# Kernel optimization log

Hardware: AMD Instinct MI355X
Metric: run time of the kernel (lower is better)

Reference implementation:

```python
import math
import jax, jax.numpy as jnp
import numpy as np

B, S, D_MODEL, NUM_HEADS = 4, 2048, 1024, 16
D_N = D_MODEL // NUM_HEADS  # 64


def setup_inputs() -> dict:
    key = jax.random.key(0)
    ks = jax.random.split(key, 10)
    scale = 1.0 / math.sqrt(D_MODEL)
    return {
        "q": jax.random.normal(ks[0], (B, S, D_MODEL), dtype=jnp.float32),
        "k": jax.random.normal(ks[1], (B, S, D_MODEL), dtype=jnp.float32),
        "v": jax.random.normal(ks[2], (B, S, D_MODEL), dtype=jnp.float32),
        "mask": jax.random.uniform(ks[3], (B, S, S), dtype=jnp.float32),
        "w_q": jax.random.normal(ks[4], (D_N, D_MODEL), dtype=jnp.float32) * scale,
        "b_q": jnp.zeros((D_N,), dtype=jnp.float32),
        "w_k": jax.random.normal(ks[5], (D_N, D_MODEL), dtype=jnp.float32) * scale,
        "b_k": jnp.zeros((D_N,), dtype=jnp.float32),
        "w_v": jax.random.normal(ks[6], (D_N, D_MODEL), dtype=jnp.float32) * scale,
        "b_v": jnp.zeros((D_N,), dtype=jnp.float32),
    }


def reference(q, k, v, mask, w_q, b_q, w_k, b_k, w_v, b_v):
    # Linear projections d_model -> d_n (torch Linear: x @ W.T + b)
    qp = jnp.einsum("bsd,nd->bsn", q, w_q) + b_q  # [B,S,d_n]
    kp = jnp.einsum("bsd,nd->bsn", k, w_k) + b_k
    vp = jnp.einsum("bsd,nd->bsn", v, w_v) + b_v
    # Scaled dot-product scores with additive mask penalty
    scores = jnp.einsum("bqn,bkn->bqk", qp, kp) / math.sqrt(D_N) + mask * (-1e9)
    attn = jax.nn.softmax(scores, axis=-1)  # [B,S,S]
    return jnp.einsum("bqk,bkn->bqn", attn, vp)  # [B,S,d_n]
```

## Files before the change

### kernel.cpp

```cpp
#include <hip/hip_runtime.h>
#include <hip/hip_bf16.h>

#define BB 4
#define SS 2048
#define DM 1024
#define DN 64

typedef short short8 __attribute__((ext_vector_type(8)));
typedef float f32x4 __attribute__((ext_vector_type(4)));
typedef unsigned short ushort;

__device__ __forceinline__ ushort f2bf(float f) {
    union { float f; unsigned u; } v; v.f = f;
    unsigned r = v.u + 0x7fffu + ((v.u >> 16) & 1u);
    return (ushort)(r >> 16);
}
__device__ __forceinline__ float bf2f(ushort h) {
    union { unsigned u; float f; } v; v.u = ((unsigned)h) << 16; return v.f;
}

__global__ __launch_bounds__(256) void prep_w(
    const float* __restrict__ wq, const float* __restrict__ wk,
    const float* __restrict__ wv, ushort* __restrict__ w_bf)
{
    int i = blockIdx.x * 256 + threadIdx.x;
    int p = i >> 14;
    int j = (i & 16383) * 4;
    const float* src = (p == 0) ? wq : (p == 1) ? wk : wv;
    float4 f = *(const float4*)(src + j);
    ushort o[4] = { f2bf(f.x), f2bf(f.y), f2bf(f.z), f2bf(f.w) };
    *(unsigned long long*)(w_bf + p * 65536 + j) = *(unsigned long long*)o;
}

__global__ __launch_bounds__(128, 2) void proj_kernel(
    const float* __restrict__ q, const float* __restrict__ k, const float* __restrict__ v,
    const ushort* __restrict__ w_bf,
    const float* __restrict__ bq, const float* __restrict__ bk, const float* __restrict__ bvp,
    ushort* __restrict__ qp, ushort* __restrict__ kp, ushort* __restrict__ vpT)
{
    const int tid  = threadIdx.x;
    const int proj = blockIdx.y;
    const int wv_id = tid >> 6;
    const int lane  = tid & 63;
    const int l16   = lane & 15;
    const int quad  = lane >> 4;
    const int g     = blockIdx.x * 2 + wv_id;
    const int m0    = g * 16;

    const float* x     = (proj == 0) ? q  : (proj == 1) ? k  : v;
    const ushort* wb   = w_bf + proj * 65536;
    const float* bias  = (proj == 0) ? bq : (proj == 1) ? bk : bvp;

    const float* arow = x + (size_t)(m0 + l16) * DM + quad * 8;

    f32x4 acc[4];
#pragma unroll
    for (int t = 0; t < 4; t++) acc[t] = (f32x4){0.f, 0.f, 0.f, 0.f};

#pragma unroll 4
    for (int kb = 0; kb < DM; kb += 32) {
        float4 f0 = *(const float4*)(arow + kb);
        float4 f1 = *(const float4*)(arow + kb + 4);
        ushort ta[8] = { f2bf(f0.x), f2bf(f0.y), f2bf(f0.z), f2bf(f0.w),
                         f2bf(f1.x), f2bf(f1.y), f2bf(f1.z), f2bf(f1.w) };
        short8 a = *(short8*)ta;
#pragma unroll
        for (int t = 0; t < 4; t++) {
            short8 b = *(const short8*)(wb + (size_t)(t * 16 + l16) * DM + kb + quad * 8);
            acc[t] = __builtin_amdgcn_mfma_f32_16x16x32_bf16(a, b, acc[t], 0, 0, 0);
        }
    }

#pragma unroll
    for (int t = 0; t < 4; t++) {
        int n = t * 16 + l16;
        float bb_ = bias[n];
#pragma unroll
        for (int r = 0; r < 4; r++) {
            int grow = m0 + quad * 4 + r;
            ushort h = f2bf(acc[t][r] + bb_);
            if (proj == 0)      qp[(size_t)grow * DN + n] = h;
            else if (proj == 1) kp[(size_t)grow * DN + n] = h;
            else {
                int bb = grow >> 11, s = grow & 2047;
                vpT[((size_t)bb * DN + n) * SS + s] = h;
            }
        }
    }
}

template<int KPS>
__global__ __launch_bounds__(256, 2) void flash_kernel(
    const float* __restrict__ mask,
    const ushort* __restrict__ qp,
    const ushort* __restrict__ kp,
    const ushort* __restrict__ vpT,
    ushort* __restrict__ part_O,
    float* __restrict__ part_ml)
{
    constexpr int NSLICE = SS / KPS;
    constexpr int NIT    = KPS / 64;

    __shared__ __align__(16) ushort p_lds[4][16][72];

    const int tid  = threadIdx.x;
    const int wv   = tid >> 6;
    const int lane = tid & 63;
    const int l16  = lane & 15;
    const int quad = lane >> 4;

    const int gw    = blockIdx.x * 4 + wv;
    const int qg    = gw & 127;
    const int rest  = gw >> 7;
    const int slice = rest % NSLICE;
    const int b     = rest / NSLICE;

    const ushort* qbase = qp + ((size_t)b * SS + qg * 16 + l16) * DN + quad * 8;
    short8 aq0 = *(const short8*)(qbase);
    short8 aq1 = *(const short8*)(qbase + 32);

    float m_r[4] = { -__builtin_inff(), -__builtin_inff(),
                     -__builtin_inff(), -__builtin_inff() };
    float l_r[4] = { 0.f, 0.f, 0.f, 0.f };
    f32x4 Oacc[4];
#pragma unroll
    for (int t = 0; t < 4; t++) Oacc[t] = (f32x4){0.f, 0.f, 0.f, 0.f};

    const size_t mrow0 = ((size_t)b * SS + qg * 16 + quad * 4) * SS;
    const int k_begin = slice * KPS;

    float  mk[2][4][4];
    short8 bk0[2][4], bk1[2][4];

    auto load_tile = [&](int buf, int k0) {
#pragma unroll
        for (int t = 0; t < 4; t++) {
            const ushort* kb_ = kp + ((size_t)b * SS + k0 + t * 16 + l16) * DN + quad * 8;
            bk0[buf][t] = *(const short8*)(kb_);
            bk1[buf][t] = *(const short8*)(kb_ + 32);
        }
#pragma unroll
        for (int t = 0; t < 4; t++)
#pragma unroll
            for (int r = 0; r < 4; r++)
                mk[buf][t][r] = mask[mrow0 + (size_t)r * SS + k0 + t * 16 + l16];
    };

    load_tile(0, k_begin);

#pragma unroll
    for (int it = 0; it < NIT; ++it) {
        const int cur = it & 1;
        const int k0  = k_begin + it * 64;

        if (it + 1 < NIT) load_tile(cur ^ 1, k0 + 64);

        short8 bv0[4], bv1[4];
#pragma unroll
        for (int tf = 0; tf < 4; tf++) {
            const ushort* vb_ = vpT + ((size_t)b * DN + tf * 16 + l16) * SS + k0 + quad * 8;
            bv0[tf] = *(const short8*)(vb_);
            bv1[tf] = *(const short8*)(vb_ + 32);
        }

        f32x4 sc[4];
#pragma unroll
        for (int t = 0; t < 4; t++) {
            f32x4 z = (f32x4){0.f, 0.f, 0.f, 0.f};
            z = __builtin_amdgcn_mfma_f32_16x16x32_bf16(aq0, bk0[cur][t], z, 0, 0, 0);
            z = __builtin_amdgcn_mfma_f32_16x16x32_bf16(aq1, bk1[cur][t], z, 0, 0, 0);
            sc[t] = z;
        }

#pragma unroll
        for (int r = 0; r < 4; r++) {
            float s[4];
            float tmax = -__builtin_inff();
#pragma unroll
            for (int t = 0; t < 4; t++) {
                s[t] = sc[t][r] * 0.125f - 1e9f * mk[cur][t][r];
                tmax = fmaxf(tmax, s[t]);
            }
#pragma unroll
            for (int off = 8; off >= 1; off >>= 1)
                tmax = fmaxf(tmax, __shfl_xor(tmax, off, 16));
            float mnew  = fmaxf(m_r[r], tmax);
            float alpha = __expf(m_r[r] - mnew);
            m_r[r] = mnew;
            float rs = 0.f;
#pragma unroll
            for (int t = 0; t < 4; t++) {
                float pv = __expf(s[t] - mnew);
                rs += pv;
                p_lds[wv][quad * 4 + r][t * 16 + l16] = f2bf(pv);
            }
#pragma unroll
            for (int off = 8; off >= 1; off >>= 1)
                rs += __shfl_xor(rs, off, 16);
            l_r[r] = l_r[r] * alpha + rs;
#pragma unroll
            for (int tf = 0; tf < 4; tf++)
                Oacc[tf][r] *= alpha;
        }

        short8 ap0 = *(const short8*)&p_lds[wv][l16][quad * 8];
        short8 ap1 = *(const short8*)&p_lds[wv][l16][32 + quad * 8];
#pragma unroll
        for (int tf = 0; tf < 4; tf++) {
            Oacc[tf] = __builtin_amdgcn_mfma_f32_16x16x32_bf16(ap0, bv0[tf], Oacc[tf], 0, 0, 0);
            Oacc[tf] = __builtin_amdgcn_mfma_f32_16x16x32_bf16(ap1, bv1[tf], Oacc[tf], 0, 0, 0);
        }
    }

    const int rowg = (b * SS + qg * 16) + quad * 4;
#pragma unroll
    for (int r = 0; r < 4; r++) {
        size_t row = (size_t)rowg + r;
        if (l16 == 0) {
            part_ml[((size_t)slice * (BB * SS) + row) * 2 + 0] = m_r[r];
            part_ml[((size_t)slice * (BB * SS) + row) * 2 + 1] = l_r[r];
        }
#pragma unroll
        for (int tf = 0; tf < 4; tf++)
            part_O[((size_t)slice * (BB * SS) + row) * DN + tf * 16 + l16] =
                f2bf(Oacc[tf][r]);
    }
}

__global__ __launch_bounds__(256) void combine_kernel(
    const ushort* __restrict__ part_O, const float* __restrict__ part_ml,
    float* __restrict__ out, int nslice)
{
    const int tid = threadIdx.x;
    const int row = blockIdx.x * 4 + (tid >> 6);
    const int f   = tid & 63;

    float ms[8], ls[8];
    float M = -__builtin_inff();
    for (int i = 0; i < nslice; i++) {
        ms[i] = part_ml[((size_t)i * (BB * SS) + row) * 2 + 0];
        ls[i] = part_ml[((size_t)i * (BB * SS) + row) * 2 + 1];
        M = fmaxf(M, ms[i]);
    }
    float L = 0.f, acc = 0.f;
    for (int i = 0; i < nslice; i++) {
        float e = __expf(ms[i] - M);
        L += e * ls[i];
        acc += e * bf2f(part_O[((size_t)i * (BB * SS) + row) * DN + f]);
    }
    out[(size_t)row * DN + f] = acc / L;
}

extern "C" void kernel_launch(void* const* d_in, const int* in_sizes, int n_in,
                              void* d_out, int out_size, void* d_ws, size_t ws_size,
                              hipStream_t stream) {
    const float* q    = (const float*)d_in[0];
    const float* k    = (const float*)d_in[1];
    const float* v    = (const float*)d_in[2];
    const float* mask = (const float*)d_in[3];
    const float* wq   = (const float*)d_in[4];
    const float* bq   = (const float*)d_in[5];
    const float* wk   = (const float*)d_in[6];
    const float* bk   = (const float*)d_in[7];
    const float* wv   = (const float*)d_in[8];
    const float* bv   = (const float*)d_in[9];
    float* out = (float*)d_out;

    char* p = (char*)d_ws;
    ushort* w_bf = (ushort*)p;                 p += 3 * 65536 * sizeof(ushort);
    ushort* qp   = (ushort*)p;                 p += (size_t)BB * SS * DN * 2;
    ushort* kp   = (ushort*)p;                 p += (size_t)BB * SS * DN * 2;
    ushort* vpT  = (ushort*)p;                 p += (size_t)BB * SS * DN * 2;
    size_t fixed = (size_t)(p - (char*)d_ws);

    int split = 8;
    while (split > 1 &&
           fixed + (size_t)split * ((size_t)BB * SS * 2 * 4 + (size_t)BB * SS * DN * 2) > ws_size)
        split >>= 1;

    float*  part_ml = (float*)p;               p += (size_t)split * BB * SS * 2 * 4;
    ushort* part_O  = (ushort*)p;

    prep_w<<<192, 256, 0, stream>>>(wq, wk, wv, w_bf);
    proj_kernel<<<dim3(256, 3), 128, 0, stream>>>(q, k, v, w_bf, bq, bk, bv, qp, kp, vpT);
    switch (split) {
        case 8:  flash_kernel<256> <<<128 * 8, 256, 0, stream>>>(mask, qp, kp, vpT, part_O, part_ml); break;
        case 4:  flash_kernel<512> <<<128 * 4, 256, 0, stream>>>(mask, qp, kp, vpT, part_O, part_ml); break;
        case 2:  flash_kernel<1024><<<128 * 2, 256, 0, stream>>>(mask, qp, kp, vpT, part_O, part_ml); break;
        default: flash_kernel<2048><<<128 * 1, 256, 0, stream>>>(mask, qp, kp, vpT, part_O, part_ml); break;
    }
    combine_kernel<<<(BB * SS) / 4, 256, 0, stream>>>(part_O, part_ml, out, split);
}
```

Measured before the change: 240.1 us.

## Fuse split-K combine into flash kernel and drop weight prep kernel

Removes the separate weight bf16 conversion kernel: the projection kernel now reads fp32 weights directly, truncates them to bf16, and software-prefetches its A and B operands. The flash kernel now assigns four key slices to the four waves of one block. It stages mask tiles through LDS with coalesced float4 loads and merges the partial softmax results in shared memory, so the partial-output buffers and the combine kernel are gone. The goal is fewer launches, less global traffic for partials, and better mask load coalescing. The cost is fewer flash blocks (512), which lowers parallelism, plus truncation rounding on the weights.

```diff
diff --git a/kernel.cpp b/kernel.cpp
--- a/kernel.cpp
+++ b/kernel.cpp
@@ -15,59 +15,95 @@
     unsigned r = v.u + 0x7fffu + ((v.u >> 16) & 1u);
     return (ushort)(r >> 16);
 }
-__device__ __forceinline__ float bf2f(ushort h) {
-    union { unsigned u; float f; } v; v.u = ((unsigned)h) << 16; return v.f;
-}
-
-__global__ __launch_bounds__(256) void prep_w(
-    const float* __restrict__ wq, const float* __restrict__ wk,
-    const float* __restrict__ wv, ushort* __restrict__ w_bf)
-{
-    int i = blockIdx.x * 256 + threadIdx.x;
-    int p = i >> 14;
-    int j = (i & 16383) * 4;
-    const float* src = (p == 0) ? wq : (p == 1) ? wk : wv;
-    float4 f = *(const float4*)(src + j);
-    ushort o[4] = { f2bf(f.x), f2bf(f.y), f2bf(f.z), f2bf(f.w) };
-    *(unsigned long long*)(w_bf + p * 65536 + j) = *(unsigned long long*)o;
-}
-
-__global__ __launch_bounds__(128, 2) void proj_kernel(
+__device__ __forceinline__ ushort f2bf_t(float f) {
+    union { float f; unsigned u; } v; v.f = f;
+    return (ushort)(v.u >> 16);
+}
+__device__ __forceinline__ short8 cvt8_rtn(float4 a, float4 b) {
+    ushort t[8] = { f2bf(a.x), f2bf(a.y), f2bf(a.z), f2bf(a.w),
+                    f2bf(b.x), f2bf(b.y), f2bf(b.z), f2bf(b.w) };
+    return *(short8*)t;
+}
+__device__ __forceinline__ short8 cvt8_trc(float4 a, float4 b) {
+    ushort t[8] = { f2bf_t(a.x), f2bf_t(a.y), f2bf_t(a.z), f2bf_t(a.w),
+                    f2bf_t(b.x), f2bf_t(b.y), f2bf_t(b.z), f2bf_t(b.w) };
+    return *(short8*)t;
+}
+
+__global__ __launch_bounds__(256) void proj_kernel(
     const float* __restrict__ q, const float* __restrict__ k, const float* __restrict__ v,
-    const ushort* __restrict__ w_bf,
+    const float* __restrict__ wq, const float* __restrict__ wk, const float* __restrict__ wvm,
     const float* __restrict__ bq, const float* __restrict__ bk, const float* __restrict__ bvp,
     ushort* __restrict__ qp, ushort* __restrict__ kp, ushort* __restrict__ vpT)
 {
-    const int tid  = threadIdx.x;
-    const int proj = blockIdx.y;
+    const int tid   = threadIdx.x;
     const int wv_id = tid >> 6;
     const int lane  = tid & 63;
     const int l16   = lane & 15;
     const int quad  = lane >> 4;
-    const int g     = blockIdx.x * 2 + wv_id;
-    const int m0    = g * 16;
-
-    const float* x     = (proj == 0) ? q  : (proj == 1) ? k  : v;
-    const ushort* wb   = w_bf + proj * 65536;
-    const float* bias  = (proj == 0) ? bq : (proj == 1) ? bk : bvp;
+    const int w     = blockIdx.x * 4 + wv_id;
+    const int proj  = w >> 9;
+    const int m0    = (w & 511) << 4;
+
+    const float* x    = (proj == 0) ? q  : (proj == 1) ? k  : v;
+    const float* wm   = (proj == 0) ? wq : (proj == 1) ? wk : wvm;
+    const float* bias = (proj == 0) ? bq : (proj == 1) ? bk : bvp;
 
     const float* arow = x + (size_t)(m0 + l16) * DM + quad * 8;
+    const float* brow0 = wm + (size_t)(l16     ) * DM + quad * 8;
+    const float* brow1 = wm + (size_t)(l16 + 16) * DM + quad * 8;
+    const float* brow2 = wm + (size_t)(l16 + 32) * DM + quad * 8;
+    const float* brow3 = wm + (size_t)(l16 + 48) * DM + quad * 8;
+
+    float4 apf[4][2];
+    float4 bpf[2][4][2];
+#pragma unroll
+    for (int i = 0; i < 4; i++) {
+        apf[i][0] = *(const float4*)(arow + i * 32);
+        apf[i][1] = *(const float4*)(arow + i * 32 + 4);
+    }
+#pragma unroll
+    for (int i = 0; i < 2; i++) {
+        bpf[i][0][0] = *(const float4*)(brow0 + i * 32);
+        bpf[i][0][1] = *(const float4*)(brow0 + i * 32 + 4);
+        bpf[i][1][0] = *(const float4*)(brow1 + i * 32);
+        bpf[i][1][1] = *(const float4*)(brow1 + i * 32 + 4);
+        bpf[i][2][0] = *(const float4*)(brow2 + i * 32);
+        bpf[i][2][1] = *(const float4*)(brow2 + i * 32 + 4);
+        bpf[i][3][0] = *(const float4*)(brow3 + i * 32);
+        bpf[i][3][1] = *(const float4*)(brow3 + i * 32 + 4);
+    }
 
     f32x4 acc[4];
 #pragma unroll
     for (int t = 0; t < 4; t++) acc[t] = (f32x4){0.f, 0.f, 0.f, 0.f};
 
-#pragma unroll 4
-    for (int kb = 0; kb < DM; kb += 32) {
-        float4 f0 = *(const float4*)(arow + kb);
-        float4 f1 = *(const float4*)(arow + kb + 4);
-        ushort ta[8] = { f2bf(f0.x), f2bf(f0.y), f2bf(f0.z), f2bf(f0.w),
-                         f2bf(f1.x), f2bf(f1.y), f2bf(f1.z), f2bf(f1.w) };
-        short8 a = *(short8*)ta;
-#pragma unroll
-        for (int t = 0; t < 4; t++) {
-            short8 b = *(const short8*)(wb + (size_t)(t * 16 + l16) * DM + kb + quad * 8);
-            acc[t] = __builtin_amdgcn_mfma_f32_16x16x32_bf16(a, b, acc[t], 0, 0, 0);
+#pragma unroll
+    for (int c = 0; c < 32; c++) {
+        const int ai = c & 3, bi = c & 1;
+        short8 a  = cvt8_rtn(apf[ai][0], apf[ai][1]);
+        short8 b0 = cvt8_trc(bpf[bi][0][0], bpf[bi][0][1]);
+        short8 b1 = cvt8_trc(bpf[bi][1][0], bpf[bi][1][1]);
+        short8 b2 = cvt8_trc(bpf[bi][2][0], bpf[bi][2][1]);
+        short8 b3 = cvt8_trc(bpf[bi][3][0], bpf[bi][3][1]);
+        acc[0] = __builtin_amdgcn_mfma_f32_16x16x32_bf16(a, b0, acc[0], 0, 0, 0);
+        acc[1] = __builtin_amdgcn_mfma_f32_16x16x32_bf16(a, b1, acc[1], 0, 0, 0);
+        acc[2] = __builtin_amdgcn_mfma_f32_16x16x32_bf16(a, b2, acc[2], 0, 0, 0);
+        acc[3] = __builtin_amdgcn_mfma_f32_16x16x32_bf16(a, b3, acc[3], 0, 0, 0);
+        if (c + 4 < 32) {
+            apf[ai][0] = *(const float4*)(arow + (c + 4) * 32);
+            apf[ai][1] = *(const float4*)(arow + (c + 4) * 32 + 4);
+        }
+        if (c + 2 < 32) {
+            const int kb = (c + 2) * 32;
+            bpf[bi][0][0] = *(const float4*)(brow0 + kb);
+            bpf[bi][0][1] = *(const float4*)(brow0 + kb + 4);
+            bpf[bi][1][0] = *(const float4*)(brow1 + kb);
+            bpf[bi][1][1] = *(const float4*)(brow1 + kb + 4);
+            bpf[bi][2][0] = *(const float4*)(brow2 + kb);
+            bpf[bi][2][1] = *(const float4*)(brow2 + kb + 4);
+            bpf[bi][3][0] = *(const float4*)(brow3 + kb);
+            bpf[bi][3][1] = *(const float4*)(brow3 + kb + 4);
         }
     }
 
@@ -82,42 +118,53 @@
             if (proj == 0)      qp[(size_t)grow * DN + n] = h;
             else if (proj == 1) kp[(size_t)grow * DN + n] = h;
             else {
-                int bb = grow >> 11, s = grow & 2047;
-                vpT[((size_t)bb * DN + n) * SS + s] = h;
+                int bb = grow >> 11, ss = grow & 2047;
+                vpT[((size_t)bb * DN + n) * SS + ss] = h;
             }
         }
     }
 }
 
-template<int KPS>
 __global__ __launch_bounds__(256, 2) void flash_kernel(
     const float* __restrict__ mask,
     const ushort* __restrict__ qp,
     const ushort* __restrict__ kp,
     const ushort* __restrict__ vpT,
-    ushort* __restrict__ part_O,
-    float* __restrict__ part_ml)
+    float* __restrict__ out)
 {
-    constexpr int NSLICE = SS / KPS;
-    constexpr int NIT    = KPS / 64;
-
-    __shared__ __align__(16) ushort p_lds[4][16][72];
+    __shared__ __align__(16) char smem[4 * 6656];
 
     const int tid  = threadIdx.x;
     const int wv   = tid >> 6;
     const int lane = tid & 63;
     const int l16  = lane & 15;
     const int quad = lane >> 4;
-
-    const int gw    = blockIdx.x * 4 + wv;
-    const int qg    = gw & 127;
-    const int rest  = gw >> 7;
-    const int slice = rest % NSLICE;
-    const int b     = rest / NSLICE;
+    const int b    = blockIdx.x >> 7;
+    const int qg   = blockIdx.x & 127;
+
+    float*  maskb = (float*)(smem + wv * 6656);
+    ushort* pbuf  = (ushort*)(smem + wv * 6656 + 4352);
+
+    const int k_begin = wv * 512;
 
     const ushort* qbase = qp + ((size_t)b * SS + qg * 16 + l16) * DN + quad * 8;
     short8 aq0 = *(const short8*)(qbase);
     short8 aq1 = *(const short8*)(qbase + 32);
+
+    const int mrow = lane >> 2;
+    const int mseg = lane & 3;
+    const float* mg = mask + ((size_t)b * SS + qg * 16 + mrow) * SS + mseg * 4;
+    float4 mpf[4];
+#pragma unroll
+    for (int j = 0; j < 4; j++) mpf[j] = *(const float4*)(mg + k_begin + j * 16);
+
+    short8 bk0[4], bk1[4];
+#pragma unroll
+    for (int t = 0; t < 4; t++) {
+        const ushort* p_ = kp + ((size_t)b * SS + k_begin + t * 16 + l16) * DN + quad * 8;
+        bk0[t] = *(const short8*)p_;
+        bk1[t] = *(const short8*)(p_ + 32);
+    }
 
     float m_r[4] = { -__builtin_inff(), -__builtin_inff(),
                      -__builtin_inff(), -__builtin_inff() };
@@ -126,59 +173,51 @@
 #pragma unroll
     for (int t = 0; t < 4; t++) Oacc[t] = (f32x4){0.f, 0.f, 0.f, 0.f};
 
-    const size_t mrow0 = ((size_t)b * SS + qg * 16 + quad * 4) * SS;
-    const int k_begin = slice * KPS;
-
-    float  mk[2][4][4];
-    short8 bk0[2][4], bk1[2][4];
-
-    auto load_tile = [&](int buf, int k0) {
-#pragma unroll
-        for (int t = 0; t < 4; t++) {
-            const ushort* kb_ = kp + ((size_t)b * SS + k0 + t * 16 + l16) * DN + quad * 8;
-            bk0[buf][t] = *(const short8*)(kb_);
-            bk1[buf][t] = *(const short8*)(kb_ + 32);
-        }
-#pragma unroll
-        for (int t = 0; t < 4; t++)
-#pragma unroll
-            for (int r = 0; r < 4; r++)
-                mk[buf][t][r] = mask[mrow0 + (size_t)r * SS + k0 + t * 16 + l16];
-    };
-
-    load_tile(0, k_begin);
-
-#pragma unroll
-    for (int it = 0; it < NIT; ++it) {
-        const int cur = it & 1;
-        const int k0  = k_begin + it * 64;
-
-        if (it + 1 < NIT) load_tile(cur ^ 1, k0 + 64);
+#pragma unroll
+    for (int it = 0; it < 8; ++it) {
+        const int k0 = k_begin + it * 64;
+
+#pragma unroll
+        for (int j = 0; j < 4; j++)
+            *(float4*)(maskb + mrow * 68 + j * 16 + mseg * 4) = mpf[j];
+        if (it < 7) {
+#pragma unroll
+            for (int j = 0; j < 4; j++) mpf[j] = *(const float4*)(mg + k0 + 64 + j * 16);
+        }
 
         short8 bv0[4], bv1[4];
 #pragma unroll
         for (int tf = 0; tf < 4; tf++) {
-            const ushort* vb_ = vpT + ((size_t)b * DN + tf * 16 + l16) * SS + k0 + quad * 8;
-            bv0[tf] = *(const short8*)(vb_);
-            bv1[tf] = *(const short8*)(vb_ + 32);
+            const ushort* p_ = vpT + ((size_t)b * DN + tf * 16 + l16) * SS + k0 + quad * 8;
+            bv0[tf] = *(const short8*)p_;
+            bv1[tf] = *(const short8*)(p_ + 32);
         }
 
         f32x4 sc[4];
 #pragma unroll
         for (int t = 0; t < 4; t++) {
             f32x4 z = (f32x4){0.f, 0.f, 0.f, 0.f};
-            z = __builtin_amdgcn_mfma_f32_16x16x32_bf16(aq0, bk0[cur][t], z, 0, 0, 0);
-            z = __builtin_amdgcn_mfma_f32_16x16x32_bf16(aq1, bk1[cur][t], z, 0, 0, 0);
+            z = __builtin_amdgcn_mfma_f32_16x16x32_bf16(aq0, bk0[t], z, 0, 0, 0);
+            z = __builtin_amdgcn_mfma_f32_16x16x32_bf16(aq1, bk1[t], z, 0, 0, 0);
             sc[t] = z;
         }
+        if (it < 7) {
+#pragma unroll
+            for (int t = 0; t < 4; t++) {
+                const ushort* p_ = kp + ((size_t)b * SS + k0 + 64 + t * 16 + l16) * DN + quad * 8;
+                bk0[t] = *(const short8*)p_;
+                bk1[t] = *(const short8*)(p_ + 32);
+            }
+        }
 
 #pragma unroll
         for (int r = 0; r < 4; r++) {
+            const float* mrow_l = maskb + (quad * 4 + r) * 68;
             float s[4];
             float tmax = -__builtin_inff();
 #pragma unroll
             for (int t = 0; t < 4; t++) {
-                s[t] = sc[t][r] * 0.125f - 1e9f * mk[cur][t][r];
+                s[t] = sc[t][r] * 0.125f - 1e9f * mrow_l[t * 16 + l16];
                 tmax = fmaxf(tmax, s[t]);
             }
 #pragma unroll
@@ -192,7 +231,7 @@
             for (int t = 0; t < 4; t++) {
                 float pv = __expf(s[t] - mnew);
                 rs += pv;
-                p_lds[wv][quad * 4 + r][t * 16 + l16] = f2bf(pv);
+                pbuf[(quad * 4 + r) * 72 + t * 16 + l16] = f2bf(pv);
             }
 #pragma unroll
             for (int off = 8; off >= 1; off >>= 1)
@@ -203,8 +242,8 @@
                 Oacc[tf][r] *= alpha;
         }
 
-        short8 ap0 = *(const short8*)&p_lds[wv][l16][quad * 8];
-        short8 ap1 = *(const short8*)&p_lds[wv][l16][32 + quad * 8];
+        short8 ap0 = *(const short8*)&pbuf[l16 * 72 + quad * 8];
+        short8 ap1 = *(const short8*)&pbuf[l16 * 72 + 32 + quad * 8];
 #pragma unroll
         for (int tf = 0; tf < 4; tf++) {
             Oacc[tf] = __builtin_amdgcn_mfma_f32_16x16x32_bf16(ap0, bv0[tf], Oacc[tf], 0, 0, 0);
@@ -212,43 +251,44 @@
         }
     }
 
-    const int rowg = (b * SS + qg * 16) + quad * 4;
-#pragma unroll
-    for (int r = 0; r < 4; r++) {
-        size_t row = (size_t)rowg + r;
-        if (l16 == 0) {
-            part_ml[((size_t)slice * (BB * SS) + row) * 2 + 0] = m_r[r];
-            part_ml[((size_t)slice * (BB * SS) + row) * 2 + 1] = l_r[r];
-        }
-#pragma unroll
-        for (int tf = 0; tf < 4; tf++)
-            part_O[((size_t)slice * (BB * SS) + row) * DN + tf * 16 + l16] =
-                f2bf(Oacc[tf][r]);
-    }
-}
-
-__global__ __launch_bounds__(256) void combine_kernel(
-    const ushort* __restrict__ part_O, const float* __restrict__ part_ml,
-    float* __restrict__ out, int nslice)
-{
-    const int tid = threadIdx.x;
-    const int row = blockIdx.x * 4 + (tid >> 6);
-    const int f   = tid & 63;
-
-    float ms[8], ls[8];
-    float M = -__builtin_inff();
-    for (int i = 0; i < nslice; i++) {
-        ms[i] = part_ml[((size_t)i * (BB * SS) + row) * 2 + 0];
-        ls[i] = part_ml[((size_t)i * (BB * SS) + row) * 2 + 1];
-        M = fmaxf(M, ms[i]);
-    }
-    float L = 0.f, acc = 0.f;
-    for (int i = 0; i < nslice; i++) {
-        float e = __expf(ms[i] - M);
-        L += e * ls[i];
-        acc += e * bf2f(part_O[((size_t)i * (BB * SS) + row) * DN + f]);
-    }
-    out[(size_t)row * DN + f] = acc / L;
+    float* Ob  = (float*)(smem + wv * 6656);
+    float* mlb = (float*)(smem + wv * 6656 + 4096);
+#pragma unroll
+    for (int tf = 0; tf < 4; tf++)
+#pragma unroll
+        for (int r = 0; r < 4; r++)
+            Ob[(quad * 4 + r) * 64 + tf * 16 + l16] = Oacc[tf][r];
+    if (l16 == 0) {
+#pragma unroll
+        for (int r = 0; r < 4; r++) {
+            mlb[(quad * 4 + r) * 2 + 0] = m_r[r];
+            mlb[(quad * 4 + r) * 2 + 1] = l_r[r];
+        }
+    }
+    __syncthreads();
+
+#pragma unroll
+    for (int j = 0; j < 4; j++) {
+        int idx = tid + j * 256;
+        int qq = idx >> 6, nn = idx & 63;
+        float ms[4], ls[4];
+        float M = -__builtin_inff();
+#pragma unroll
+        for (int s = 0; s < 4; s++) {
+            const float* ml_s = (const float*)(smem + s * 6656 + 4096);
+            ms[s] = ml_s[qq * 2 + 0];
+            ls[s] = ml_s[qq * 2 + 1];
+            M = fmaxf(M, ms[s]);
+        }
+        float L = 0.f, accv = 0.f;
+#pragma unroll
+        for (int s = 0; s < 4; s++) {
+            float e = __expf(ms[s] - M);
+            L += e * ls[s];
+            accv += e * ((const float*)(smem + s * 6656))[qq * 64 + nn];
+        }
+        out[((size_t)b * SS + qg * 16 + qq) * DN + nn] = accv / L;
+    }
 }
 
 extern "C" void kernel_launch(void* const* d_in, const int* in_sizes, int n_in,
@@ -267,27 +307,10 @@
     float* out = (float*)d_out;
 
     char* p = (char*)d_ws;
-    ushort* w_bf = (ushort*)p;                 p += 3 * 65536 * sizeof(ushort);
-    ushort* qp   = (ushort*)p;                 p += (size_t)BB * SS * DN * 2;
-    ushort* kp   = (ushort*)p;                 p += (size_t)BB * SS * DN * 2;
-    ushort* vpT  = (ushort*)p;                 p += (size_t)BB * SS * DN * 2;
-    size_t fixed = (size_t)(p - (char*)d_ws);
-
-    int split = 8;
-    while (split > 1 &&
-           fixed + (size_t)split * ((size_t)BB * SS * 2 * 4 + (size_t)BB * SS * DN * 2) > ws_size)
-        split >>= 1;
-
-    float*  part_ml = (float*)p;               p += (size_t)split * BB * SS * 2 * 4;
-    ushort* part_O  = (ushort*)p;
-
-    prep_w<<<192, 256, 0, stream>>>(wq, wk, wv, w_bf);
-    proj_kernel<<<dim3(256, 3), 128, 0, stream>>>(q, k, v, w_bf, bq, bk, bv, qp, kp, vpT);
-    switch (split) {
-        case 8:  flash_kernel<256> <<<128 * 8, 256, 0, stream>>>(mask, qp, kp, vpT, part_O, part_ml); break;
-        case 4:  flash_kernel<512> <<<128 * 4, 256, 0, stream>>>(mask, qp, kp, vpT, part_O, part_ml); break;
-        case 2:  flash_kernel<1024><<<128 * 2, 256, 0, stream>>>(mask, qp, kp, vpT, part_O, part_ml); break;
-        default: flash_kernel<2048><<<128 * 1, 256, 0, stream>>>(mask, qp, kp, vpT, part_O, part_ml); break;
-    }
-    combine_kernel<<<(BB * SS) / 4, 256, 0, stream>>>(part_O, part_ml, out, split);
-}
+    ushort* qp  = (ushort*)p;   p += (size_t)BB * SS * DN * 2;
+    ushort* kp  = (ushort*)p;   p += (size_t)BB * SS * DN * 2;
+    ushort* vpT = (ushort*)p;
+
+    proj_kernel<<<384, 256, 0, stream>>>(q, k, v, wq, wk, wv, bq, bk, bv, qp, kp, vpT);
+    flash_kernel<<<BB * 128, 256, 0, stream>>>(mask, qp, kp, vpT, out);
+}
```

Measured after the change: 253.2 us. 5.5% more time.
